# Performance work log

Measured on AMD Instinct MI355X. Metric: run time of the kernel, lower is better.

The kernel has to match this reference:

```python
import jax, jax.numpy as jnp
import numpy as np

N, C, T, V = 16, 256, 256, 64   # batch, node_channel_in, time, total_nodes
SC, SV = 3, 64                  # node_channel_out, num_seeds
NEW_NODES, C_OUT = 64, 3
IN_DIM = C * V + SC * SV        # 16576


def setup_inputs() -> dict:
    key = jax.random.key(0)
    k1, k2, k3, k4 = jax.random.split(key, 4)
    x = jax.random.normal(k1, (N, C, T, V), dtype=jnp.float32)
    seeds = jax.random.normal(k2, (N, T, SC, SV), dtype=jnp.float32)
    # Stacked weights of the `new_nodes` independent Linear(IN_DIM, C_OUT) layers
    W = jax.random.normal(k3, (NEW_NODES, C_OUT, IN_DIM), dtype=jnp.float32) * 0.02
    b = jax.random.normal(k4, (NEW_NODES, C_OUT), dtype=jnp.float32) * 0.02
    return {"x": x, "seeds": seeds, "W": W, "b": b}


def reference(x, seeds, W, b):
    n, c, t, v = x.shape
    # (n,c,t,v) -> (n,t,c*v)
    xm = jnp.transpose(x, (0, 2, 1, 3)).reshape(n, t, c * v)
    sm = seeds.reshape(n, t, -1)                 # (n,t,sc*sv)
    mix = jnp.concatenate([xm, sm], axis=2)      # (n,t,IN_DIM)
    # Fused horizontal GEMM over all new_nodes projections, then stacked on dim 3:
    # out[n,t,c_out,j] = sum_k mix[n,t,k] * W[j,c_out,k] + b[j,c_out]
    out = jnp.einsum('ntk,jck->ntcj', mix, W) + b.T[None, None]
    return out  # (n, t, node_channel_out, new_nodes)
```

## Files before the change

### kernel.cpp

```cpp
#include <hip/hip_runtime.h>
#include <hip/hip_bf16.h>

typedef unsigned short u16;
typedef unsigned int   u32;
typedef __attribute__((ext_vector_type(8))) short bf16x8;
typedef __attribute__((ext_vector_type(4))) float f32x4;

#define NB    16
#define CIN   256
#define TDIM  256
#define VDIM  64
#define PCOL  192
#define NCHX  256
#define NCH   259
#define MTOT  4096
#define CHUNK_U16 12288
#define WT_BYTES ((size_t)NCH * CHUNK_U16 * 2)

__device__ __forceinline__ u16 f2bf(float f) {
  u32 u = __builtin_bit_cast(u32, f);
  u32 r = u + 0x7fffu + ((u >> 16) & 1u);
  return (u16)(r >> 16);
}
__device__ __forceinline__ u32 pk2(float a, float b) {
  return (u32)f2bf(a) | ((u32)f2bf(b) << 16);
}
__device__ __forceinline__ void gload_lds16(const void* g, void* l) {
  __builtin_amdgcn_global_load_lds(
      (const __attribute__((address_space(1))) u32*)g,
      (__attribute__((address_space(3))) u32*)l, 16, 0, 0);
}

__global__ void prep_w(const float* __restrict__ W, u16* __restrict__ Wt) {
  int u  = blockIdx.x * 256 + threadIdx.x;
  int q  = u & 7;
  int p  = (u >> 3) % PCOL;
  int ch = u / (PCOL * 8);
  int j = p & 63, co = p >> 6;
  const float* src = W + (size_t)(j * 3 + co) * 16576 + ch * 64 + q * 8;
  float4 fa = *(const float4*)src;
  float4 fb = *(const float4*)(src + 4);
  uint4 v;
  v.x = pk2(fa.x, fa.y); v.y = pk2(fa.z, fa.w);
  v.z = pk2(fb.x, fb.y); v.w = pk2(fb.z, fb.w);
  ((uint4*)Wt)[(size_t)ch * 1536 + p * 8 + (q ^ (p & 7))] = v;
}

__global__ __launch_bounds__(512, 4)
void gemm_bf16(const float* __restrict__ x, const float* __restrict__ seeds,
               const u16* __restrict__ Wt, float* __restrict__ dst,
               const float* __restrict__ bias, int S) {
  __shared__ __align__(16) u16 lds[2][16384];
  const int tid  = threadIdx.x;
  const int lane = tid & 63;
  const int wid  = tid >> 6;
  const int wm   = wid >> 2;
  const int wn   = wid & 3;
  const int bid  = blockIdx.x;
  int mblk, ksp;
  if (S == 8) { ksp = bid & 7;  mblk = bid >> 3; }
  else        { mblk = bid & 63; ksp = bid >> 6; }
  const int n  = mblk >> 2;
  const int t0 = (mblk & 3) << 6;
  const int c0 = (NCH * ksp) / S;
  const int c1 = (NCH * (ksp + 1)) / S;

  const int q0 = tid & 7;
  const int m0 = tid >> 3;
  const int lr = lane & 15, lq = lane >> 4;

  f32x4 acc[2][3] = {};

  struct ASet { float4 ra, rb; };
  ASet AX, AY;

  auto Bi = [&](int ch, int buf) {
    const char* gsrc = (const char*)Wt + (size_t)ch * 24576 + wid * 3072 + lane * 16;
    char* lbase = (char*)&lds[buf][4096] + wid * 3072;
    #pragma unroll
    for (int r = 0; r < 3; ++r)
      gload_lds16(gsrc + (size_t)r * 1024, lbase + r * 1024);
  };
  auto Ai = [&](int ch, ASet& s) {
    const float* a0;
    if (ch < NCHX)
      a0 = x + (((size_t)n * CIN + ch) * TDIM + (t0 + m0)) * VDIM + q0 * 8;
    else
      a0 = seeds + ((size_t)n * TDIM + (t0 + m0)) * 192 + (ch - NCHX) * 64 + q0 * 8;
    s.ra = *(const float4*)a0; s.rb = *(const float4*)(a0 + 4);
  };
  auto CONV = [&](const ASet& s, int buf) {
    uint4 v;
    v.x = pk2(s.ra.x, s.ra.y); v.y = pk2(s.ra.z, s.ra.w);
    v.z = pk2(s.rb.x, s.rb.y); v.w = pk2(s.rb.z, s.rb.w);
    ((uint4*)&lds[buf][0])[m0 * 8 + (q0 ^ (m0 & 7))] = v;
  };

  auto COMPUTE = [&](int buf) {
    const u16* L = &lds[buf][0];
    #pragma unroll
    for (int ks = 0; ks < 2; ++ks) {
      const int q = ks * 4 + lq;
      bf16x8 af[2], bfr[3];
      #pragma unroll
      for (int mt = 0; mt < 2; ++mt) {
        int m = wm * 32 + mt * 16 + lr;
        af[mt] = *(const bf16x8*)(L + (m * 8 + (q ^ (m & 7))) * 8);
      }
      #pragma unroll
      for (int nt = 0; nt < 3; ++nt) {
        int p = wn * 48 + nt * 16 + lr;
        bfr[nt] = *(const bf16x8*)(L + 4096 + (p * 8 + (q ^ (p & 7))) * 8);
      }
      #pragma unroll
      for (int mt = 0; mt < 2; ++mt)
        #pragma unroll
        for (int nt = 0; nt < 3; ++nt)
          acc[mt][nt] = __builtin_amdgcn_mfma_f32_16x16x32_bf16(
              af[mt], bfr[nt], acc[mt][nt], 0, 0, 0);
    }
  };

  Bi(c0, 0);
  Ai(c0, AX);
  if (c0 + 1 < c1) { Bi(c0 + 1, 1); Ai(c0 + 1, AY); }
  __builtin_amdgcn_sched_barrier(0);
  CONV(AX, 0);
  asm volatile("s_waitcnt lgkmcnt(0)" ::: "memory");
  __builtin_amdgcn_sched_barrier(0);
  __builtin_amdgcn_s_barrier();
  __builtin_amdgcn_sched_barrier(0);

#define PHASE(PAR, AP, AN)                                                    \
  {                                                                           \
    COMPUTE(PAR);                                                             \
    const bool hasN  = (ch + 1 < c1);                                         \
    const bool hasNN = (ch + 2 < c1);                                         \
    if (!hasN) break;                                                         \
    asm volatile("s_waitcnt lgkmcnt(0)" ::: "memory");                        \
    __builtin_amdgcn_sched_barrier(0);                                        \
    __builtin_amdgcn_s_barrier();                \
    __builtin_amdgcn_sched_barrier(0);                                        \
    if (hasNN) { Bi(ch + 2, PAR); Ai(ch + 2, AN); }                           \
    __builtin_amdgcn_sched_barrier(0);                                        \
    CONV(AP, (PAR) ^ 1);        \
    asm volatile("s_waitcnt lgkmcnt(0)" ::: "memory");                        \
    __builtin_amdgcn_sched_barrier(0);                                        \
    __builtin_amdgcn_s_barrier();                               \
    __builtin_amdgcn_sched_barrier(0);                                        \
  }

  int ch = c0;
  while (true) {
    PHASE(0, AY, AX)
    ++ch;
    PHASE(1, AX, AY)
    ++ch;
  }
#undef PHASE

  float* dbase = dst + (size_t)ksp * MTOT * PCOL;
  #pragma unroll
  for (int mt = 0; mt < 2; ++mt)
    #pragma unroll
    for (int nt = 0; nt < 3; ++nt) {
      int col = wn * 48 + nt * 16 + lr;
      float bv = bias ? bias[(col & 63) * 3 + (col >> 6)] : 0.f;
      #pragma unroll
      for (int r = 0; r < 4; ++r) {
        int row = mblk * 64 + wm * 32 + mt * 16 + lq * 4 + r;
        dbase[(size_t)row * PCOL + col] = acc[mt][nt][r] + bv;
      }
    }
}

__global__ void reduce_k(const float* __restrict__ part, const float* __restrict__ b,
                         float* __restrict__ out, int S) {
  int i4 = (blockIdx.x * 256 + threadIdx.x) * 4;
  float4 a = *(const float4*)&part[i4];
  for (int s = 1; s < S; ++s) {
    const float4 v = *(const float4*)&part[(size_t)s * (MTOT * PCOL) + i4];
    a.x += v.x; a.y += v.y; a.z += v.z; a.w += v.w;
  }
  int p0 = i4 % PCOL;
  a.x += b[((p0 + 0) & 63) * 3 + ((p0 + 0) >> 6)];
  a.y += b[((p0 + 1) & 63) * 3 + ((p0 + 1) >> 6)];
  a.z += b[((p0 + 2) & 63) * 3 + ((p0 + 2) >> 6)];
  a.w += b[((p0 + 3) & 63) * 3 + ((p0 + 3) >> 6)];
  *(float4*)&out[i4] = a;
}

__global__ void fallback_k(const float* __restrict__ x, const float* __restrict__ seeds,
                           const float* __restrict__ W, const float* __restrict__ b,
                           float* __restrict__ out) {
  __shared__ float mk[512];
  int m = blockIdx.x, n = m >> 8, t = m & 255, p = threadIdx.x;
  float acc = 0.f;
  for (int k0 = 0; k0 < 16576; k0 += 512) {
    int kn = min(512, 16576 - k0);
    __syncthreads();
    for (int i = threadIdx.x; i < kn; i += 256) {
      int k = k0 + i;
      mk[i] = (k < 16384)
                ? x[(((size_t)n * 256 + (k >> 6)) * 256 + t) * 64 + (k & 63)]
                : seeds[((size_t)n * 256 + t) * 192 + (k - 16384)];
    }
    __syncthreads();
    if (p < PCOL) {
      const float* wr = W + (size_t)((p & 63) * 3 + (p >> 6)) * 16576 + k0;
      for (int i = 0; i < kn; ++i) acc += mk[i] * wr[i];
    }
  }
  if (p < PCOL) out[(size_t)m * PCOL + p] = acc + b[(p & 63) * 3 + (p >> 6)];
}

extern "C" void kernel_launch(void* const* d_in, const int* in_sizes, int n_in,
                              void* d_out, int out_size, void* d_ws, size_t ws_size,
                              hipStream_t stream) {
  (void)in_sizes; (void)n_in; (void)out_size;
  const float* x     = (const float*)d_in[0];
  const float* seeds = (const float*)d_in[1];
  const float* W     = (const float*)d_in[2];
  const float* b     = (const float*)d_in[3];
  float* out = (float*)d_out;

  if (ws_size < WT_BYTES) {
    fallback_k<<<dim3(MTOT), dim3(256), 0, stream>>>(x, seeds, W, b, out);
    return;
  }
  u16* Wt = (u16*)d_ws;
  int S = 8;
  while (S > 1 && WT_BYTES + (size_t)S * MTOT * PCOL * 4 > ws_size) S >>= 1;
  if (WT_BYTES + (size_t)S * MTOT * PCOL * 4 > ws_size) S = 1;

  prep_w<<<dim3((NCH * PCOL * 8) / 256), dim3(256), 0, stream>>>(W, Wt);
  if (S == 1) {
    gemm_bf16<<<dim3(64), dim3(512), 0, stream>>>(x, seeds, Wt, out, b, 1);
  } else {
    float* part = (float*)((char*)d_ws + WT_BYTES);
    gemm_bf16<<<dim3(64 * S), dim3(512), 0, stream>>>(x, seeds, Wt, part, nullptr, S);
    reduce_k<<<dim3(MTOT * PCOL / 4 / 256), dim3(256), 0, stream>>>(part, b, out, S);
  }
}
```

Baseline: 81.24 us.

## Process two K-chunks per pipeline stage and halve split-K factor

Each pipeline stage now loads and converts two 64-wide K-chunks into a doubled LDS buffer, computing both before a barrier, which halves the number of block-wide barriers per K range. Split-K drops from 8 to 4, so each block covers a longer K range, the partial buffer shrinks, and the reduce pass reads less. Launch bounds fall to 2 blocks per CU because of the larger LDS footprint. Grid size halves to 256 blocks, so there is less parallelism and occupancy, and each thread holds more A-chunk registers in flight.

Measured after the change: 92.20 us. 13.5% more time.

```diff
diff --git a/kernel.cpp b/kernel.cpp
--- a/kernel.cpp
+++ b/kernel.cpp
@@ -46,11 +46,11 @@
   ((uint4*)Wt)[(size_t)ch * 1536 + p * 8 + (q ^ (p & 7))] = v;
 }
 
-__global__ __launch_bounds__(512, 4)
+__global__ __launch_bounds__(512, 2)
 void gemm_bf16(const float* __restrict__ x, const float* __restrict__ seeds,
                const u16* __restrict__ Wt, float* __restrict__ dst,
                const float* __restrict__ bias, int S) {
-  __shared__ __align__(16) u16 lds[2][16384];
+  __shared__ __align__(16) u16 lds[2][32768];
   const int tid  = threadIdx.x;
   const int lane = tid & 63;
   const int wid  = tid >> 6;
@@ -58,7 +58,7 @@
   const int wn   = wid & 3;
   const int bid  = blockIdx.x;
   int mblk, ksp;
-  if (S == 8) { ksp = bid & 7;  mblk = bid >> 3; }
+  if (S == 4) { ksp = bid & 3;  mblk = bid >> 2; }
   else        { mblk = bid & 63; ksp = bid >> 6; }
   const int n  = mblk >> 2;
   const int t0 = (mblk & 3) << 6;
@@ -71,46 +71,60 @@
 
   f32x4 acc[2][3] = {};
 
-  struct ASet { float4 ra, rb; };
+  struct ASet { float4 a0, b0, a1, b1; };
   ASet AX, AY;
 
-  auto Bi = [&](int ch, int buf) {
-    const char* gsrc = (const char*)Wt + (size_t)ch * 24576 + wid * 3072 + lane * 16;
-    char* lbase = (char*)&lds[buf][4096] + wid * 3072;
+  auto arow = [&](int ch) -> const float* {
+    if (ch < NCHX)
+      return x + (((size_t)n * CIN + ch) * TDIM + (t0 + m0)) * VDIM + q0 * 8;
+    return seeds + ((size_t)n * TDIM + (t0 + m0)) * 192 + (ch - NCHX) * 64 + q0 * 8;
+  };
+  auto Ai = [&](int cc, ASet& s) {
+    const float* a = arow(cc);
+    s.a0 = *(const float4*)a; s.b0 = *(const float4*)(a + 4);
+    if (cc + 1 < c1) {
+      const float* b = arow(cc + 1);
+      s.a1 = *(const float4*)b; s.b1 = *(const float4*)(b + 4);
+    }
+  };
+  auto Bi = [&](int cc, int buf) {
     #pragma unroll
-    for (int r = 0; r < 3; ++r)
-      gload_lds16(gsrc + (size_t)r * 1024, lbase + r * 1024);
-  };
-  auto Ai = [&](int ch, ASet& s) {
-    const float* a0;
-    if (ch < NCHX)
-      a0 = x + (((size_t)n * CIN + ch) * TDIM + (t0 + m0)) * VDIM + q0 * 8;
-    else
-      a0 = seeds + ((size_t)n * TDIM + (t0 + m0)) * 192 + (ch - NCHX) * 64 + q0 * 8;
-    s.ra = *(const float4*)a0; s.rb = *(const float4*)(a0 + 4);
-  };
-  auto CONV = [&](const ASet& s, int buf) {
+    for (int s = 0; s < 2; ++s) {
+      if (cc + s >= c1) break;
+      const char* gsrc = (const char*)Wt + (size_t)(cc + s) * 24576 + wid * 3072 + lane * 16;
+      char* lb = (char*)&lds[buf][0] + 16384 + s * 24576 + wid * 3072;
+      #pragma unroll
+      for (int r = 0; r < 3; ++r)
+        gload_lds16(gsrc + (size_t)r * 1024, lb + r * 1024);
+    }
+  };
+  auto CONV = [&](const ASet& s, int buf, int cc) {
     uint4 v;
-    v.x = pk2(s.ra.x, s.ra.y); v.y = pk2(s.ra.z, s.ra.w);
-    v.z = pk2(s.rb.x, s.rb.y); v.w = pk2(s.rb.z, s.rb.w);
+    v.x = pk2(s.a0.x, s.a0.y); v.y = pk2(s.a0.z, s.a0.w);
+    v.z = pk2(s.b0.x, s.b0.y); v.w = pk2(s.b0.z, s.b0.w);
     ((uint4*)&lds[buf][0])[m0 * 8 + (q0 ^ (m0 & 7))] = v;
-  };
-
-  auto COMPUTE = [&](int buf) {
+    if (cc + 1 < c1) {
+      v.x = pk2(s.a1.x, s.a1.y); v.y = pk2(s.a1.z, s.a1.w);
+      v.z = pk2(s.b1.x, s.b1.y); v.w = pk2(s.b1.z, s.b1.w);
+      ((uint4*)&lds[buf][4096])[m0 * 8 + (q0 ^ (m0 & 7))] = v;
+    }
+  };
+
+  auto CHALF = [&](int buf, int sub) {
     const u16* L = &lds[buf][0];
     #pragma unroll
-    for (int ks = 0; ks < 2; ++ks) {
-      const int q = ks * 4 + lq;
+    for (int kq = 0; kq < 2; ++kq) {
+      const int q = kq * 4 + lq;
       bf16x8 af[2], bfr[3];
       #pragma unroll
       for (int mt = 0; mt < 2; ++mt) {
         int m = wm * 32 + mt * 16 + lr;
-        af[mt] = *(const bf16x8*)(L + (m * 8 + (q ^ (m & 7))) * 8);
+        af[mt] = *(const bf16x8*)(L + sub * 4096 + (m * 8 + (q ^ (m & 7))) * 8);
       }
       #pragma unroll
       for (int nt = 0; nt < 3; ++nt) {
         int p = wn * 48 + nt * 16 + lr;
-        bfr[nt] = *(const bf16x8*)(L + 4096 + (p * 8 + (q ^ (p & 7))) * 8);
+        bfr[nt] = *(const bf16x8*)(L + 8192 + sub * 12288 + (p * 8 + (q ^ (p & 7))) * 8);
       }
       #pragma unroll
       for (int mt = 0; mt < 2; ++mt)
@@ -123,9 +137,9 @@
 
   Bi(c0, 0);
   Ai(c0, AX);
-  if (c0 + 1 < c1) { Bi(c0 + 1, 1); Ai(c0 + 1, AY); }
+  if (c0 + 2 < c1) { Bi(c0 + 2, 1); Ai(c0 + 2, AY); }
   __builtin_amdgcn_sched_barrier(0);
-  CONV(AX, 0);
+  CONV(AX, 0, c0);
   asm volatile("s_waitcnt lgkmcnt(0)" ::: "memory");
   __builtin_amdgcn_sched_barrier(0);
   __builtin_amdgcn_s_barrier();
@@ -133,29 +147,30 @@
 
 #define PHASE(PAR, AP, AN)                                                    \
   {                                                                           \
-    COMPUTE(PAR);                                                             \
-    const bool hasN  = (ch + 1 < c1);                                         \
-    const bool hasNN = (ch + 2 < c1);                                         \
+    CHALF(PAR, 0);                                                            \
+    if (cc + 1 < c1) CHALF(PAR, 1);                                           \
+    const bool hasN  = (cc + 2 < c1);                                         \
+    const bool hasNN = (cc + 4 < c1);                                         \
     if (!hasN) break;                                                         \
     asm volatile("s_waitcnt lgkmcnt(0)" ::: "memory");                        \
     __builtin_amdgcn_sched_barrier(0);                                        \
-    __builtin_amdgcn_s_barrier();                \
-    __builtin_amdgcn_sched_barrier(0);                                        \
-    if (hasNN) { Bi(ch + 2, PAR); Ai(ch + 2, AN); }                           \
-    __builtin_amdgcn_sched_barrier(0);                                        \
-    CONV(AP, (PAR) ^ 1);        \
+    __builtin_amdgcn_s_barrier();                  \
+    __builtin_amdgcn_sched_barrier(0);                                        \
+    if (hasNN) { Bi(cc + 4, PAR); Ai(cc + 4, AN); }                           \
+    __builtin_amdgcn_sched_barrier(0);                                        \
+    CONV(AP, (PAR) ^ 1, cc + 2);    \
     asm volatile("s_waitcnt lgkmcnt(0)" ::: "memory");                        \
     __builtin_amdgcn_sched_barrier(0);                                        \
     __builtin_amdgcn_s_barrier();                               \
     __builtin_amdgcn_sched_barrier(0);                                        \
   }
 
-  int ch = c0;
+  int cc = c0;
   while (true) {
     PHASE(0, AY, AX)
-    ++ch;
+    cc += 2;
     PHASE(1, AX, AY)
-    ++ch;
+    cc += 2;
   }
 #undef PHASE
 
@@ -229,7 +244,7 @@
     return;
   }
   u16* Wt = (u16*)d_ws;
-  int S = 8;
+  int S = 4;
   while (S > 1 && WT_BYTES + (size_t)S * MTOT * PCOL * 4 > ws_size) S >>= 1;
   if (WT_BYTES + (size_t)S * MTOT * PCOL * 4 > ws_size) S = 1;
 
```
